# Kernel optimization log

Measured on AMD Instinct MI355X. Metric: run time of the kernel, lower is better.

## Reference

```python
import jax, jax.numpy as jnp
import numpy as np

B = 16384      # batch of Monte Carlo paths
N = 100        # time steps
DIM_W = 3
DT = 0.01
SQRT_DT = DT ** 0.5
SIGMA0 = 0.5   # constant diffusion coefficient (concrete sigma = SIGMA0 * ones(B,1,DIM_W))


def _mlp(x, W1, b1, W2, b2, W3, b3):
    h = jax.nn.relu(x @ W1 + b1)
    h = jax.nn.relu(h @ W2 + b2)
    return h @ W3 + b3


def setup_inputs() -> dict:
    key = jax.random.key(0)
    ks = jax.random.split(key, 8)
    s = 0.1  # modest weight scale for numerical sanity
    return {
        'y0': jnp.ones((1,), jnp.float32),
        'Y0': jnp.zeros((1, 1), jnp.float32),
        'zW1': s * jax.random.normal(ks[0], (2, 64), jnp.float32),
        'zb1': jnp.zeros((64,), jnp.float32),
        'zW2': s * jax.random.normal(ks[1], (64, 64), jnp.float32),
        'zb2': jnp.zeros((64,), jnp.float32),
        'zW3': s * jax.random.normal(ks[2], (64, 3), jnp.float32),
        'zb3': jnp.zeros((3,), jnp.float32),
        'qW1': s * jax.random.normal(ks[3], (2, 64), jnp.float32),
        'qb1': jnp.zeros((64,), jnp.float32),
        'qW2': s * jax.random.normal(ks[4], (64, 64), jnp.float32),
        'qb2': jnp.zeros((64,), jnp.float32),
        'qW3': s * jax.random.normal(ks[5], (64, 1), jnp.float32),
        'qb3': jnp.zeros((1,), jnp.float32),
        'dW': jax.random.normal(ks[6], (N, B, DIM_W), jnp.float32),
        'dZ': jax.random.normal(ks[7], (N, B, DIM_W), jnp.float32),
    }


def reference(y0, Y0, zW1, zb1, zW2, zb2, zW3, zb3,
              qW1, qb1, qW2, qb2, qW3, qb3, dW, dZ):
    y = jnp.broadcast_to(y0.reshape(1, 1), (B, 1))          # (B,1) state
    Y = jnp.broadcast_to(Y0, (B, 1))                         # (B,1) value process
    t = jnp.zeros((B, 1), jnp.float32)

    def step(carry, noise):
        y, Y, t, loss_acc = carry
        dWi, dZi = noise
        inp = jnp.concatenate([t, y], axis=1)                # (B,2)
        z = _mlp(inp, zW1, zb1, zW2, zb2, zW3, zb3)          # (B,3)
        q = _mlp(inp, qW1, qb1, qW2, qb2, qW3, qb3)          # (B,1)
        f = 0.5 * q * q                                      # generator (B,1)
        dw = dWi * SQRT_DT
        dz = dZi * SQRT_DT
        # sigma = SIGMA0 * ones(B,1,DIM_W); bmm(sigma, dw) = SIGMA0 * sum_j dw_j
        diffusion = SIGMA0 * jnp.sum(dw, axis=1, keepdims=True)
        y_new = y + q * DT + diffusion                       # mu = q
        Y_next = Y - f * DT + jnp.sum(z * dw, axis=1, keepdims=True)
        residual = Y_next - (Y - f * DT + jnp.sum(z * dz, axis=1, keepdims=True))
        loss_acc = loss_acc + jnp.mean(residual * residual)
        return (y_new, Y_next, t + DT, loss_acc), None

    (y, Y, t, total_residual_loss), _ = jax.lax.scan(
        step, (y, Y, t, jnp.float32(0.0)), (dW, dZ))
    terminal = y * y                                         # terminal_cost(y)
    terminal_loss = jnp.mean((Y - terminal) ** 2)
    return terminal_loss + total_residual_loss
```

## Files before the change

kernel.cpp:

```cpp
#include <hip/hip_runtime.h>
#include <hip/hip_bf16.h>

#define BATCH   16384
#define NSTEPS  100
#define DT_     0.01f
#define SQRTDT  0.1f
#define SIGMA0_ 0.5f

typedef _Float16  f16x2  __attribute__((ext_vector_type(2)));
typedef _Float16  f16x4  __attribute__((ext_vector_type(4)));
typedef _Float16  f16x8  __attribute__((ext_vector_type(8)));
typedef __fp16    h16x2  __attribute__((ext_vector_type(2)));
typedef float     f32x4  __attribute__((ext_vector_type(4)));

typedef const __attribute__((address_space(1))) void* gas_ptr;
typedef __attribute__((address_space(3))) void*       las_ptr;

__global__ void zero_out_kernel(float* out) { if (threadIdx.x == 0) out[0] = 0.0f; }

static __device__ __forceinline__ f16x4 pk4(const f32x4& d) {
    union { h16x2 h[2]; f16x4 v; } c;
    c.h[0] = __builtin_amdgcn_cvt_pkrtz(d[0], d[1]);
    c.h[1] = __builtin_amdgcn_cvt_pkrtz(d[2], d[3]);
    return c.v;
}

__launch_bounds__(256, 1)
__global__ void deepbsde_kernel(
    const float* __restrict__ y0,  const float* __restrict__ Y0,
    const float* __restrict__ zW1, const float* __restrict__ zb1,
    const float* __restrict__ zW2, const float* __restrict__ zb2,
    const float* __restrict__ zW3, const float* __restrict__ zb3,
    const float* __restrict__ qW1, const float* __restrict__ qb1,
    const float* __restrict__ qW2, const float* __restrict__ qb2,
    const float* __restrict__ qW3, const float* __restrict__ qb3,
    const float* __restrict__ dW,  const float* __restrict__ dZ,
    float* __restrict__ out)
{
    __shared__ __align__(16) char ring[4][8][384];
    __shared__ __align__(16) _Float16 tbl[NSTEPS * 128];

    const int tid  = threadIdx.x;
    const int lane = tid & 63;
    const int w    = tid >> 6;
    const int ln15 = lane & 15, q4 = lane >> 4;
    const int gw   = (blockIdx.x << 2) + w;
    const int pbase = gw << 4;

    auto fill = [&](int i) {
        if (lane < 24) {
            const char* g = (lane < 12)
                ? (const char*)dW + ((size_t)i * BATCH + pbase) * 12 + (size_t)lane * 16
                : (const char*)dZ + ((size_t)i * BATCH + pbase) * 12 + (size_t)(lane - 12) * 16;
            __builtin_amdgcn_global_load_lds((gas_ptr)g, (las_ptr)&ring[w][i & 7][0],
                                             16, 0, 0);
        }
    };
    fill(0); fill(1); fill(2); fill(3);

    {
        float tt = 0.0f;
        for (int i = 0; i < NSTEPS; ++i) {
            int r = (tid - (i << 6)) & 255;
            if (r < 64) {
                int q4e = r >> 4, mlp = (r >> 3) & 1, m = r & 7;
                const float* Wp = mlp ? qW1 : zW1;
                const float* bp = mlp ? qb1 : zb1;
                int i0 = 2*m, i1 = 2*m + 1;
                int k0 = 32*(i0 >> 3) + 8*q4e + (i0 & 7);
                int k1 = 32*(i1 >> 3) + 8*q4e + (i1 & 7);
                _Float16 th = (_Float16)tt;
                f16x2 A = {(_Float16)Wp[k0], (_Float16)Wp[k1]};
                f16x2 C = {(_Float16)bp[k0], (_Float16)bp[k1]};
                f16x2 tv = {th, th};
                f16x2 v = A*tv + C;
                int idx = (i*4 + q4e)*16 + mlp*8 + m;
                *(f16x2*)&tbl[idx << 1] = v;
            }
            tt += DT_;
        }
    }

    f16x2 B1z[8], B1q[8];
#pragma unroll
    for (int m = 0; m < 8; ++m) {
        int i0 = 2*m, i1 = 2*m + 1;
        int k0 = 32*(i0 >> 3) + 8*q4 + (i0 & 7);
        int k1 = 32*(i1 >> 3) + 8*q4 + (i1 & 7);
        B1z[m] = (f16x2){(_Float16)zW1[64 + k0], (_Float16)zW1[64 + k1]};
        B1q[m] = (f16x2){(_Float16)qW1[64 + k0], (_Float16)qW1[64 + k1]};
    }

    f16x8 AfZ[4][2], AfQ[4][2];
#pragma unroll
    for (int tN = 0; tN < 4; ++tN)
#pragma unroll
        for (int f = 0; f < 2; ++f)
#pragma unroll
            for (int j = 0; j < 8; ++j) {
                int k = 32*f + 8*q4 + j, n = 16*tN + ln15;
                AfZ[tN][f][j] = (_Float16)zW2[k*64 + n];
                AfQ[tN][f][j] = (_Float16)qW2[k*64 + n];
            }

    f32x4 b2zv[4], b2qv[4];
#pragma unroll
    for (int tN = 0; tN < 4; ++tN)
#pragma unroll
        for (int r = 0; r < 4; ++r) {
            b2zv[tN][r] = zb2[16*tN + 4*q4 + r];
            b2qv[tN][r] = qb2[16*tN + 4*q4 + r];
        }

    const int c3 = ln15 & 3;
    f16x8 A3[4];
#pragma unroll
    for (int f = 0; f < 4; ++f)
#pragma unroll
        for (int j = 0; j < 8; ++j) {
            int tN = 2*(f & 1) + (j >> 2);
            int n  = 16*tN + 4*q4 + (j & 3);
            float wv = (f < 2) ? ((c3 < 3)  ? SQRTDT * zW3[n*3 + c3] : 0.0f)
                               : ((c3 == 3) ? qW3[n]                 : 0.0f);
            A3[f][j] = (_Float16)wv;
        }

    float y = y0[0], Yv = Y0[0], acc = 0.0f;
    const float CSIG = SIGMA0_ * SQRTDT;
    const float NHDT = -0.5f * DT_;
    const f32x4 C3bias = {SQRTDT * zb3[0], SQRTDT * zb3[1], SQRTDT * zb3[2], qb3[0]};

    const f16x2 zero2h = {(_Float16)0.0f, (_Float16)0.0f};
    const f16x4 zero4h = {(_Float16)0.0f, (_Float16)0.0f, (_Float16)0.0f, (_Float16)0.0f};
    const f32x4 zero4  = {0.0f, 0.0f, 0.0f, 0.0f};

    f16x8 cz0, cz1, cq0, cq1, dz0, dz1, dq0, dq1;

    auto body = [&](int i,
                    f16x8& tz0, f16x8& tz1, f16x8& tq0, f16x8& tq1,
                    f16x8& uz0, f16x8& uz1, f16x8& uq0, f16x8& uq1) {
        const float* sl = (const float*)&ring[w][i & 7][0];
        float nw0 = sl[ln15*3 + 0], nw1 = sl[ln15*3 + 1], nw2 = sl[ln15*3 + 2];
        float nz0 = sl[48 + ln15*3 + 0], nz1 = sl[48 + ln15*3 + 1], nz2 = sl[48 + ln15*3 + 2];

        int ip = i + 1; ip = (ip > NSTEPS - 1) ? NSTEPS - 1 : ip;
        {
            const f16x8* tp = (const f16x8*)(tbl + (ip*4 + q4)*32);
            uz0 = tp[0]; uz1 = tp[1]; uq0 = tp[2]; uq1 = tp[3];
        }

        _Float16 yh = (_Float16)y;
        const f16x2 yv = {yh, yh};
        union U8 { f16x8 v; f16x2 h[4]; };
        U8 Tz0; Tz0.v = tz0; U8 Tz1; Tz1.v = tz1;
        U8 Tq0; Tq0.v = tq0; U8 Tq1; Tq1.v = tq1;
        union { f16x2 h[4]; f16x8 v; } bz0, bz1, bq0, bq1;
#pragma unroll
        for (int m = 0; m < 4; ++m) {
            bz0.h[m] = __builtin_elementwise_max((f16x2)(B1z[m]*yv + Tz0.h[m]), zero2h);
            bq0.h[m] = __builtin_elementwise_max((f16x2)(B1q[m]*yv + Tq0.h[m]), zero2h);
            bz1.h[m] = __builtin_elementwise_max((f16x2)(B1z[m+4]*yv + Tz1.h[m]), zero2h);
            bq1.h[m] = __builtin_elementwise_max((f16x2)(B1q[m+4]*yv + Tq1.h[m]), zero2h);
        }

        union { f16x4 q[4]; f16x8 o[2]; } Bz, Bq;
#pragma unroll
        for (int tN = 0; tN < 4; ++tN) {
            f32x4 dz = b2zv[tN];
            dz = __builtin_amdgcn_mfma_f32_16x16x32_f16(AfZ[tN][0], bz0.v, dz, 0, 0, 0);
            dz = __builtin_amdgcn_mfma_f32_16x16x32_f16(AfZ[tN][1], bz1.v, dz, 0, 0, 0);
            f32x4 dq = b2qv[tN];
            dq = __builtin_amdgcn_mfma_f32_16x16x32_f16(AfQ[tN][0], bq0.v, dq, 0, 0, 0);
            dq = __builtin_amdgcn_mfma_f32_16x16x32_f16(AfQ[tN][1], bq1.v, dq, 0, 0, 0);
            Bz.q[tN] = __builtin_elementwise_max(pk4(dz), zero4h);
            Bq.q[tN] = __builtin_elementwise_max(pk4(dq), zero4h);
        }

        f32x4 Pz = C3bias, Pq = zero4;
        Pz = __builtin_amdgcn_mfma_f32_16x16x32_f16(A3[0], Bz.o[0], Pz, 0, 0, 0);
        Pz = __builtin_amdgcn_mfma_f32_16x16x32_f16(A3[1], Bz.o[1], Pz, 0, 0, 0);
        Pq = __builtin_amdgcn_mfma_f32_16x16x32_f16(A3[2], Bq.o[0], Pq, 0, 0, 0);
        Pq = __builtin_amdgcn_mfma_f32_16x16x32_f16(A3[3], Bq.o[1], Pq, 0, 0, 0);
        f32x4 P = Pz + Pq;

        float zs0 = P[0], zs1 = P[1], zs2 = P[2], qv = P[3];
        float zdw = fmaf(zs2, nw2, fmaf(zs1, nw1, zs0*nw0));
        float zdz = fmaf(zs2, nz2, fmaf(zs1, nz1, zs0*nz0));
        float snw = (nw0 + nw1) + nw2;
        Yv = fmaf(NHDT*qv, qv, Yv) + zdw;
        float r = zdw - zdz;
        acc = fmaf(r, r, acc);
        y = fmaf(CSIG, snw, fmaf(qv, DT_, y));
    };

    __syncthreads();
    {
        const f16x8* tp0 = (const f16x8*)(tbl + q4*32);
        cz0 = tp0[0]; cz1 = tp0[1]; cq0 = tp0[2]; cq1 = tp0[3];
    }

#pragma unroll 1
    for (int i = 0; i < NSTEPS - 4; i += 2) {
        __builtin_amdgcn_s_waitcnt(0x0F73);
        fill(i + 4);
        body(i,     cz0, cz1, cq0, cq1, dz0, dz1, dq0, dq1);
        __builtin_amdgcn_s_waitcnt(0x0F73);
        fill(i + 5);
        body(i + 1, dz0, dz1, dq0, dq1, cz0, cz1, cq0, cq1);
    }
    __builtin_amdgcn_s_waitcnt(0x0F70);
    body(NSTEPS - 4, cz0, cz1, cq0, cq1, dz0, dz1, dq0, dq1);
    body(NSTEPS - 3, dz0, dz1, dq0, dq1, cz0, cz1, cq0, cq1);
    body(NSTEPS - 2, cz0, cz1, cq0, cq1, dz0, dz1, dq0, dq1);
    body(NSTEPS - 1, dz0, dz1, dq0, dq1, cz0, cz1, cq0, cq1);

    float dterm = Yv - y*y;
    acc = fmaf(dterm, dterm, acc);

    float val = (q4 == 0) ? acc : 0.0f;
#pragma unroll
    for (int off = 1; off < 64; off <<= 1) val += __shfl_xor(val, off);
    if (lane == 0) atomicAdd(out, val * (1.0f / BATCH));
}

extern "C" void kernel_launch(void* const* d_in, const int* in_sizes, int n_in,
                              void* d_out, int out_size, void* d_ws, size_t ws_size,
                              hipStream_t stream)
{
    zero_out_kernel<<<1, 64, 0, stream>>>((float*)d_out);
    deepbsde_kernel<<<256, 256, 0, stream>>>(
        (const float*)d_in[0],  (const float*)d_in[1],
        (const float*)d_in[2],  (const float*)d_in[3],
        (const float*)d_in[4],  (const float*)d_in[5],
        (const float*)d_in[6],  (const float*)d_in[7],
        (const float*)d_in[8],  (const float*)d_in[9],
        (const float*)d_in[10], (const float*)d_in[11],
        (const float*)d_in[12], (const float*)d_in[13],
        (const float*)d_in[14], (const float*)d_in[15],
        (float*)d_out);
}
```

Baseline: 164.8 us.

## Split z and q MLPs across producer/consumer wavefronts with LDS flag handoff

Each 16-path group is now served by two wavefronts. The q-wave runs the q MLP and the y recurrence on the critical path, then passes y through an LDS ring with spin-wait flags. The z-wave consumes that y to evaluate the z MLP and the residual terms off the critical path. The grid doubles to 512 blocks and launch bounds are set to allow 2 blocks per CU. This shortens the serial per-step dependency chain, at the cost of volatile LDS spin-waits, cross-wave synchronisation overhead, and the risk of deadlock or of memory-ordering problems without fences.

```diff
diff --git a/kernel.cpp b/kernel.cpp
--- a/kernel.cpp
+++ b/kernel.cpp
@@ -25,7 +25,7 @@
     return c.v;
 }
 
-__launch_bounds__(256, 1)
+__launch_bounds__(256, 2)
 __global__ void deepbsde_kernel(
     const float* __restrict__ y0,  const float* __restrict__ Y0,
     const float* __restrict__ zW1, const float* __restrict__ zb1,
@@ -37,26 +37,42 @@
     const float* __restrict__ dW,  const float* __restrict__ dZ,
     float* __restrict__ out)
 {
-    __shared__ __align__(16) char ring[4][8][384];
+    __shared__ __align__(16) char zring[2][8][384];
+    __shared__ __align__(16) char qring[2][8][192];
     __shared__ __align__(16) _Float16 tbl[NSTEPS * 128];
+    __shared__ float yring[2][8][16];
+    __shared__ float ffin[2][16];
+    __shared__ int   flags[2][2];
 
     const int tid  = threadIdx.x;
     const int lane = tid & 63;
     const int w    = tid >> 6;
+    const int g    = w & 1;
+    const bool isQ = (w >= 2);
     const int ln15 = lane & 15, q4 = lane >> 4;
-    const int gw   = (blockIdx.x << 2) + w;
+    const int gw   = (blockIdx.x << 1) + g;
     const int pbase = gw << 4;
 
-    auto fill = [&](int i) {
+    if (tid < 4) ((int*)flags)[tid] = 0;
+
+    auto fillz = [&](int i) {
         if (lane < 24) {
-            const char* g = (lane < 12)
+            const char* gp = (lane < 12)
                 ? (const char*)dW + ((size_t)i * BATCH + pbase) * 12 + (size_t)lane * 16
                 : (const char*)dZ + ((size_t)i * BATCH + pbase) * 12 + (size_t)(lane - 12) * 16;
-            __builtin_amdgcn_global_load_lds((gas_ptr)g, (las_ptr)&ring[w][i & 7][0],
+            __builtin_amdgcn_global_load_lds((gas_ptr)gp, (las_ptr)&zring[g][i & 7][0],
                                              16, 0, 0);
         }
     };
-    fill(0); fill(1); fill(2); fill(3);
+    auto fillq = [&](int i) {
+        if (lane < 12) {
+            const char* gp = (const char*)dW + ((size_t)i * BATCH + pbase) * 12 + (size_t)lane * 16;
+            __builtin_amdgcn_global_load_lds((gas_ptr)gp, (las_ptr)&qring[g][i & 7][0],
+                                             16, 0, 0);
+        }
+    };
+    if (!isQ) { fillz(0); fillz(1); fillz(2); fillz(3); }
+    else      { fillq(0); fillq(1); fillq(2); fillq(3); }
 
     {
         float tt = 0.0f;
@@ -81,17 +97,20 @@
         }
     }
 
-    f16x2 B1z[8], B1q[8];
+    const float* W1p = isQ ? qW1 : zW1;
+    const float* W2p = isQ ? qW2 : zW2;
+    const float* b2p = isQ ? qb2 : zb2;
+
+    f16x2 B1[8];
 #pragma unroll
     for (int m = 0; m < 8; ++m) {
         int i0 = 2*m, i1 = 2*m + 1;
         int k0 = 32*(i0 >> 3) + 8*q4 + (i0 & 7);
         int k1 = 32*(i1 >> 3) + 8*q4 + (i1 & 7);
-        B1z[m] = (f16x2){(_Float16)zW1[64 + k0], (_Float16)zW1[64 + k1]};
-        B1q[m] = (f16x2){(_Float16)qW1[64 + k0], (_Float16)qW1[64 + k1]};
+        B1[m] = (f16x2){(_Float16)W1p[64 + k0], (_Float16)W1p[64 + k1]};
     }
 
-    f16x8 AfZ[4][2], AfQ[4][2];
+    f16x8 Af[4][2];
 #pragma unroll
     for (int tN = 0; tN < 4; ++tN)
 #pragma unroll
@@ -99,128 +118,168 @@
 #pragma unroll
             for (int j = 0; j < 8; ++j) {
                 int k = 32*f + 8*q4 + j, n = 16*tN + ln15;
-                AfZ[tN][f][j] = (_Float16)zW2[k*64 + n];
-                AfQ[tN][f][j] = (_Float16)qW2[k*64 + n];
+                Af[tN][f][j] = (_Float16)W2p[k*64 + n];
             }
 
-    f32x4 b2zv[4], b2qv[4];
+    f32x4 b2v[4];
 #pragma unroll
     for (int tN = 0; tN < 4; ++tN)
 #pragma unroll
-        for (int r = 0; r < 4; ++r) {
-            b2zv[tN][r] = zb2[16*tN + 4*q4 + r];
-            b2qv[tN][r] = qb2[16*tN + 4*q4 + r];
-        }
+        for (int r = 0; r < 4; ++r)
+            b2v[tN][r] = b2p[16*tN + 4*q4 + r];
 
     const int c3 = ln15 & 3;
-    f16x8 A3[4];
-#pragma unroll
-    for (int f = 0; f < 4; ++f)
+    f16x8 A3[2];
+#pragma unroll
+    for (int fl = 0; fl < 2; ++fl)
 #pragma unroll
         for (int j = 0; j < 8; ++j) {
-            int tN = 2*(f & 1) + (j >> 2);
+            int tN = 2*fl + (j >> 2);
             int n  = 16*tN + 4*q4 + (j & 3);
-            float wv = (f < 2) ? ((c3 < 3)  ? SQRTDT * zW3[n*3 + c3] : 0.0f)
-                               : ((c3 == 3) ? qW3[n]                 : 0.0f);
-            A3[f][j] = (_Float16)wv;
-        }
-
-    float y = y0[0], Yv = Y0[0], acc = 0.0f;
+            float wv = isQ ? ((c3 == 3) ? qW3[n]                 : 0.0f)
+                           : ((c3 < 3)  ? SQRTDT * zW3[n*3 + c3] : 0.0f);
+            A3[fl][j] = (_Float16)wv;
+        }
+
+    const f32x4 C3b = isQ ? (f32x4){0.0f, 0.0f, 0.0f, qb3[0]}
+                          : (f32x4){SQRTDT*zb3[0], SQRTDT*zb3[1], SQRTDT*zb3[2], 0.0f};
+
     const float CSIG = SIGMA0_ * SQRTDT;
     const float NHDT = -0.5f * DT_;
-    const f32x4 C3bias = {SQRTDT * zb3[0], SQRTDT * zb3[1], SQRTDT * zb3[2], qb3[0]};
+    const float y0v = y0[0], Y0v = Y0[0];
 
     const f16x2 zero2h = {(_Float16)0.0f, (_Float16)0.0f};
     const f16x4 zero4h = {(_Float16)0.0f, (_Float16)0.0f, (_Float16)0.0f, (_Float16)0.0f};
-    const f32x4 zero4  = {0.0f, 0.0f, 0.0f, 0.0f};
-
-    f16x8 cz0, cz1, cq0, cq1, dz0, dz1, dq0, dq1;
-
-    auto body = [&](int i,
-                    f16x8& tz0, f16x8& tz1, f16x8& tq0, f16x8& tq1,
-                    f16x8& uz0, f16x8& uz1, f16x8& uq0, f16x8& uq1) {
-        const float* sl = (const float*)&ring[w][i & 7][0];
-        float nw0 = sl[ln15*3 + 0], nw1 = sl[ln15*3 + 1], nw2 = sl[ln15*3 + 2];
-        float nz0 = sl[48 + ln15*3 + 0], nz1 = sl[48 + ln15*3 + 1], nz2 = sl[48 + ln15*3 + 2];
-
-        int ip = i + 1; ip = (ip > NSTEPS - 1) ? NSTEPS - 1 : ip;
-        {
-            const f16x8* tp = (const f16x8*)(tbl + (ip*4 + q4)*32);
-            uz0 = tp[0]; uz1 = tp[1]; uq0 = tp[2]; uq1 = tp[3];
-        }
-
-        _Float16 yh = (_Float16)y;
+
+    auto mlp = [&](float ycur, f16x8 t0, f16x8 t1) -> f32x4 {
+        _Float16 yh = (_Float16)ycur;
         const f16x2 yv = {yh, yh};
         union U8 { f16x8 v; f16x2 h[4]; };
-        U8 Tz0; Tz0.v = tz0; U8 Tz1; Tz1.v = tz1;
-        U8 Tq0; Tq0.v = tq0; U8 Tq1; Tq1.v = tq1;
-        union { f16x2 h[4]; f16x8 v; } bz0, bz1, bq0, bq1;
+        U8 T0; T0.v = t0; U8 T1; T1.v = t1;
+        union { f16x2 h[4]; f16x8 v; } b0, b1;
 #pragma unroll
         for (int m = 0; m < 4; ++m) {
-            bz0.h[m] = __builtin_elementwise_max((f16x2)(B1z[m]*yv + Tz0.h[m]), zero2h);
-            bq0.h[m] = __builtin_elementwise_max((f16x2)(B1q[m]*yv + Tq0.h[m]), zero2h);
-            bz1.h[m] = __builtin_elementwise_max((f16x2)(B1z[m+4]*yv + Tz1.h[m]), zero2h);
-            bq1.h[m] = __builtin_elementwise_max((f16x2)(B1q[m+4]*yv + Tq1.h[m]), zero2h);
-        }
-
-        union { f16x4 q[4]; f16x8 o[2]; } Bz, Bq;
+            b0.h[m] = __builtin_elementwise_max((f16x2)(B1[m]*yv   + T0.h[m]), zero2h);
+            b1.h[m] = __builtin_elementwise_max((f16x2)(B1[m+4]*yv + T1.h[m]), zero2h);
+        }
+        union { f16x4 q[4]; f16x8 o[2]; } Bh;
 #pragma unroll
         for (int tN = 0; tN < 4; ++tN) {
-            f32x4 dz = b2zv[tN];
-            dz = __builtin_amdgcn_mfma_f32_16x16x32_f16(AfZ[tN][0], bz0.v, dz, 0, 0, 0);
-            dz = __builtin_amdgcn_mfma_f32_16x16x32_f16(AfZ[tN][1], bz1.v, dz, 0, 0, 0);
-            f32x4 dq = b2qv[tN];
-            dq = __builtin_amdgcn_mfma_f32_16x16x32_f16(AfQ[tN][0], bq0.v, dq, 0, 0, 0);
-            dq = __builtin_amdgcn_mfma_f32_16x16x32_f16(AfQ[tN][1], bq1.v, dq, 0, 0, 0);
-            Bz.q[tN] = __builtin_elementwise_max(pk4(dz), zero4h);
-            Bq.q[tN] = __builtin_elementwise_max(pk4(dq), zero4h);
-        }
-
-        f32x4 Pz = C3bias, Pq = zero4;
-        Pz = __builtin_amdgcn_mfma_f32_16x16x32_f16(A3[0], Bz.o[0], Pz, 0, 0, 0);
-        Pz = __builtin_amdgcn_mfma_f32_16x16x32_f16(A3[1], Bz.o[1], Pz, 0, 0, 0);
-        Pq = __builtin_amdgcn_mfma_f32_16x16x32_f16(A3[2], Bq.o[0], Pq, 0, 0, 0);
-        Pq = __builtin_amdgcn_mfma_f32_16x16x32_f16(A3[3], Bq.o[1], Pq, 0, 0, 0);
-        f32x4 P = Pz + Pq;
-
-        float zs0 = P[0], zs1 = P[1], zs2 = P[2], qv = P[3];
-        float zdw = fmaf(zs2, nw2, fmaf(zs1, nw1, zs0*nw0));
-        float zdz = fmaf(zs2, nz2, fmaf(zs1, nz1, zs0*nz0));
-        float snw = (nw0 + nw1) + nw2;
-        Yv = fmaf(NHDT*qv, qv, Yv) + zdw;
-        float r = zdw - zdz;
-        acc = fmaf(r, r, acc);
-        y = fmaf(CSIG, snw, fmaf(qv, DT_, y));
+            f32x4 d = b2v[tN];
+            d = __builtin_amdgcn_mfma_f32_16x16x32_f16(Af[tN][0], b0.v, d, 0, 0, 0);
+            d = __builtin_amdgcn_mfma_f32_16x16x32_f16(Af[tN][1], b1.v, d, 0, 0, 0);
+            Bh.q[tN] = __builtin_elementwise_max(pk4(d), zero4h);
+        }
+        f32x4 Pv = C3b;
+        Pv = __builtin_amdgcn_mfma_f32_16x16x32_f16(A3[0], Bh.o[0], Pv, 0, 0, 0);
+        Pv = __builtin_amdgcn_mfma_f32_16x16x32_f16(A3[1], Bh.o[1], Pv, 0, 0, 0);
+        return Pv;
     };
 
     __syncthreads();
-    {
-        const f16x8* tp0 = (const f16x8*)(tbl + q4*32);
-        cz0 = tp0[0]; cz1 = tp0[1]; cq0 = tp0[2]; cq1 = tp0[3];
+
+    f16x8 c0, c1, d0, d1;
+
+    if (!isQ) {
+        float y = y0v, Ysum = 0.0f, acc = 0.0f;
+        { const f16x8* tp = (const f16x8*)(tbl + q4*32); c0 = tp[0]; c1 = tp[1]; }
+
+        auto zbody = [&](int i, f16x8& t0, f16x8& t1, f16x8& u0, f16x8& u1) {
+            const float* sl = (const float*)&zring[g][i & 7][0];
+            float nw0 = sl[ln15*3 + 0], nw1 = sl[ln15*3 + 1], nw2 = sl[ln15*3 + 2];
+            float nz0 = sl[48 + ln15*3 + 0], nz1 = sl[48 + ln15*3 + 1], nz2 = sl[48 + ln15*3 + 2];
+            int ip = i + 1; ip = (ip > NSTEPS - 1) ? NSTEPS - 1 : ip;
+            { const f16x8* tp = (const f16x8*)(tbl + (ip*4 + q4)*32); u0 = tp[0]; u1 = tp[1]; }
+
+            f32x4 P = mlp(y, t0, t1);
+            float zs0 = P[0], zs1 = P[1], zs2 = P[2];
+            float zdw = fmaf(zs2, nw2, fmaf(zs1, nw1, zs0*nw0));
+            float zdz = fmaf(zs2, nz2, fmaf(zs1, nz1, zs0*nz0));
+            Ysum += zdw;
+            float r = zdw - zdz;
+            acc = fmaf(r, r, acc);
+
+            volatile int* qf = &flags[g][0];
+            while (*qf < i + 1) { }
+            y = *(volatile float*)&yring[g][(i + 1) & 7][ln15];
+            if (lane == 0) *(volatile int*)&flags[g][1] = i + 1;
+        };
+
+#pragma unroll 1
+        for (int i = 0; i < NSTEPS - 4; i += 2) {
+            __builtin_amdgcn_s_waitcnt(0x0F73);
+            fillz(i + 4);
+            zbody(i,     c0, c1, d0, d1);
+            __builtin_amdgcn_s_waitcnt(0x0F73);
+            fillz(i + 5);
+            zbody(i + 1, d0, d1, c0, c1);
+        }
+        __builtin_amdgcn_s_waitcnt(0x0F70);
+        zbody(NSTEPS - 4, c0, c1, d0, d1);
+        zbody(NSTEPS - 3, d0, d1, c0, c1);
+        zbody(NSTEPS - 2, c0, c1, d0, d1);
+        zbody(NSTEPS - 1, d0, d1, c0, c1);
+
+        {
+            volatile int* qf = &flags[g][0];
+            while (*qf < NSTEPS + 1) { }
+        }
+        float Fq  = *(volatile float*)&ffin[g][ln15];
+        float Yvf = Y0v + Fq + Ysum;
+        float dterm = Yvf - y*y;
+        acc = fmaf(dterm, dterm, acc);
+
+        float val = (q4 == 0) ? acc : 0.0f;
+#pragma unroll
+        for (int off = 1; off < 64; off <<= 1) val += __shfl_xor(val, off);
+        if (lane == 0) atomicAdd(out, val * (1.0f / BATCH));
+    } else {
+        float y = y0v, Facc = 0.0f;
+        { const f16x8* tp = (const f16x8*)(tbl + q4*32); c0 = tp[2]; c1 = tp[3]; }
+
+        auto qbody = [&](int j, f16x8& t0, f16x8& t1, f16x8& u0, f16x8& u1) {
+            const float* sl = (const float*)&qring[g][j & 7][0];
+            float nw0 = sl[ln15*3 + 0], nw1 = sl[ln15*3 + 1], nw2 = sl[ln15*3 + 2];
+
+            f32x4 P = mlp(y, t0, t1);
+            float qv = P[3];
+
+            if (j >= 6) {
+                volatile int* zp = &flags[g][1];
+                while (*zp < j - 5) { }
+            }
+
+            float snw = (nw0 + nw1) + nw2;
+            Facc = fmaf(NHDT*qv, qv, Facc);
+            y = fmaf(CSIG, snw, fmaf(qv, DT_, y));
+
+            if (q4 == 0) *(volatile float*)&yring[g][(j + 1) & 7][ln15] = y;
+            __builtin_amdgcn_s_waitcnt(0xC07F);
+            if (lane == 0) *(volatile int*)&flags[g][0] = j + 1;
+
+            int jp = j + 1; jp = (jp > NSTEPS - 1) ? NSTEPS - 1 : jp;
+            { const f16x8* tp = (const f16x8*)(tbl + (jp*4 + q4)*32); u0 = tp[2]; u1 = tp[3]; }
+        };
+
+#pragma unroll 1
+        for (int j = 0; j < NSTEPS - 4; j += 2) {
+            __builtin_amdgcn_s_waitcnt(0x0F73);
+            fillq(j + 4);
+            qbody(j,     c0, c1, d0, d1);
+            __builtin_amdgcn_s_waitcnt(0x0F73);
+            fillq(j + 5);
+            qbody(j + 1, d0, d1, c0, c1);
+        }
+        __builtin_amdgcn_s_waitcnt(0x0F70);
+        qbody(NSTEPS - 4, c0, c1, d0, d1);
+        qbody(NSTEPS - 3, d0, d1, c0, c1);
+        qbody(NSTEPS - 2, c0, c1, d0, d1);
+        qbody(NSTEPS - 1, d0, d1, c0, c1);
+
+        if (q4 == 0) *(volatile float*)&ffin[g][ln15] = Facc;
+        __builtin_amdgcn_s_waitcnt(0xC07F);
+        if (lane == 0) *(volatile int*)&flags[g][0] = NSTEPS + 1;
     }
-
-#pragma unroll 1
-    for (int i = 0; i < NSTEPS - 4; i += 2) {
-        __builtin_amdgcn_s_waitcnt(0x0F73);
-        fill(i + 4);
-        body(i,     cz0, cz1, cq0, cq1, dz0, dz1, dq0, dq1);
-        __builtin_amdgcn_s_waitcnt(0x0F73);
-        fill(i + 5);
-        body(i + 1, dz0, dz1, dq0, dq1, cz0, cz1, cq0, cq1);
-    }
-    __builtin_amdgcn_s_waitcnt(0x0F70);
-    body(NSTEPS - 4, cz0, cz1, cq0, cq1, dz0, dz1, dq0, dq1);
-    body(NSTEPS - 3, dz0, dz1, dq0, dq1, cz0, cz1, cq0, cq1);
-    body(NSTEPS - 2, cz0, cz1, cq0, cq1, dz0, dz1, dq0, dq1);
-    body(NSTEPS - 1, dz0, dz1, dq0, dq1, cz0, cz1, cq0, cq1);
-
-    float dterm = Yv - y*y;
-    acc = fmaf(dterm, dterm, acc);
-
-    float val = (q4 == 0) ? acc : 0.0f;
-#pragma unroll
-    for (int off = 1; off < 64; off <<= 1) val += __shfl_xor(val, off);
-    if (lane == 0) atomicAdd(out, val * (1.0f / BATCH));
 }
 
 extern "C" void kernel_launch(void* const* d_in, const int* in_sizes, int n_in,
@@ -228,7 +287,7 @@
                               hipStream_t stream)
 {
     zero_out_kernel<<<1, 64, 0, stream>>>((float*)d_out);
-    deepbsde_kernel<<<256, 256, 0, stream>>>(
+    deepbsde_kernel<<<512, 256, 0, stream>>>(
         (const float*)d_in[0],  (const float*)d_in[1],
         (const float*)d_in[2],  (const float*)d_in[3],
         (const float*)d_in[4],  (const float*)d_in[5],
```

Result: no change. 165.2 us (+0.2%).
